# Performance work log

Measured on AMD Instinct MI355X. Metric: run time of the kernel, lower is better.

## Reference

```python
import jax, jax.numpy as jnp
import numpy as np

N = 50000      # nodes
E = 800000     # edges (avg degree 16)
D_IN = 128
D_H = 128
D_OUT = 8


def setup_inputs() -> dict:
    key = jax.random.key(0)
    ks = jax.random.split(key, 12)
    def lin(k, fan_in, shape):
        return (jax.random.normal(k, shape, jnp.float32) / np.float32(np.sqrt(fan_in)))
    return {
        "node_features": jax.random.normal(ks[0], (N, D_IN), jnp.float32),
        "edge_index": jax.random.randint(ks[1], (2, E), 0, N, jnp.int32),
        # 3 GCNConv layers: weight [in, out] + bias [out]
        "W0": lin(ks[2], D_IN, (D_IN, D_H)), "b0": jnp.zeros((D_H,), jnp.float32),
        "W1": lin(ks[3], D_H, (D_H, D_H)),  "b1": jnp.zeros((D_H,), jnp.float32),
        "W2": lin(ks[4], D_H, (D_H, D_H)),  "b2": jnp.zeros((D_H,), jnp.float32),
        # classifier MLP: hidden -> hidden//2 -> output
        "cW1": lin(ks[5], D_H, (D_H, D_H // 2)), "cb1": jnp.zeros((D_H // 2,), jnp.float32),
        "cW2": lin(ks[6], D_H // 2, (D_H // 2, D_OUT)), "cb2": jnp.zeros((D_OUT,), jnp.float32),
    }


def _gcn_norm(edge_index, n):
    # PyG GCNConv default: add self-loops, symmetric D^-1/2 (A+I) D^-1/2 normalization
    loops = jnp.arange(n, dtype=edge_index.dtype)
    src = jnp.concatenate([edge_index[0], loops])   # message sources j
    dst = jnp.concatenate([edge_index[1], loops])   # aggregation targets i
    deg = jax.ops.segment_sum(jnp.ones_like(src, dtype=jnp.float32), dst, num_segments=n)
    dinv = jax.lax.rsqrt(jnp.maximum(deg, 1.0))     # deg >= 1 due to self-loops
    norm = dinv[src] * dinv[dst]                    # [E+N]
    return src, dst, norm


def _gcn_conv(x, W, b, src, dst, norm, n):
    h = x @ W                                        # [N, out] dense transform first (PyG order)
    msg = h[src] * norm[:, None]                     # gather + scale  [E+N, out]
    out = jax.ops.segment_sum(msg, dst, num_segments=n)  # scatter-add
    return out + b


def reference(node_features, edge_index, W0, b0, W1, b1, W2, b2, cW1, cb1, cW2, cb2):
    n = node_features.shape[0]
    src, dst, norm = _gcn_norm(edge_index, n)
    x = jax.nn.relu(_gcn_conv(node_features, W0, b0, src, dst, norm, n))  # dropout is identity in eval
    x = jax.nn.relu(_gcn_conv(x, W1, b1, src, dst, norm, n))
    x = _gcn_conv(x, W2, b2, src, dst, norm, n)       # last conv: no relu/dropout
    # classifier MLP (dropout identity in eval)
    h = jax.nn.relu(x @ cW1 + cb1)
    return h @ cW2 + cb2                              # [N, D_OUT]
```

## Files before the change

### kernel.cpp

```cpp
#include <hip/hip_runtime.h>
#include <hip/hip_fp16.h>


#define CAP 48
#define FPG 256

using half8v  = __attribute__((ext_vector_type(8))) _Float16;
using float4v = __attribute__((ext_vector_type(4))) float;

__global__ __launch_bounds__(256) void fill_kernel(const int* __restrict__ src,
                                                   const int* __restrict__ dst, int e, int n,
                                                   const float* __restrict__ W0,
                                                   const float* __restrict__ W1,
                                                   const float* __restrict__ W2,
                                                   const float* __restrict__ cW1,
                                                   const float* __restrict__ cb1,
                                                   const float* __restrict__ b2,
                                                   int* __restrict__ cnt,
                                                   unsigned short* __restrict__ col,
                                                   __half* __restrict__ Wf0,
                                                   __half* __restrict__ Wf1,
                                                   __half* __restrict__ Wfc,
                                                   float* __restrict__ bc) {
    int b = blockIdx.x;
    int tid = threadIdx.x;
    const int FILLB = 8 * FPG;
    if (b < FILLB) {
        int g = b & 7;
        int cb = b >> 3;
        int npp = (n + 7) >> 3;
        int lo = g * npp;
        int hi = min(lo + npp, n);
        int step = FPG * 256;
        for (int i = cb * 256 + tid; i < e; i += step) {
            int d = dst[i];
            int s = src[i];
            if (d >= lo && d < hi) {
                int c = atomicAdd(&cnt[d], 1);
                if (c < CAP) col[d * CAP + c] = (unsigned short)s;
            }
        }
        return;
    }
    b -= FILLB;
    if (b < 16) {
        int t = b * 256 + tid;
        const float* W = (t < 2048) ? W0 : W1;
        __half* Wf = (t < 2048) ? Wf0 : Wf1;
        int u = t & 2047;
        int lane = u & 63, tile = (u >> 6) & 7, kk = u >> 9;
        int k0 = kk * 32 + (lane >> 4) * 8;
        int nn = tile * 16 + (lane & 15);
        __half tmp[8];
        #pragma unroll
        for (int j = 0; j < 8; j++) tmp[j] = __float2half(W[(k0 + j) * 128 + nn]);
        *(float4*)(Wf + (size_t)u * 8) = *(const float4*)tmp;
        return;
    }
    b -= 16;
    if (b < 4) {
        int u = b * 256 + tid;
        int lane = u & 63, tile = (u >> 6) & 3, kk = u >> 8;
        int k0 = kk * 32 + (lane >> 4) * 8;
        int nn = tile * 16 + (lane & 15);
        float a[8] = {};
        for (int m = 0; m < 128; m++) {
            float c = cW1[m * 64 + nn];
            #pragma unroll
            for (int j = 0; j < 8; j++) a[j] = fmaf(W2[(k0 + j) * 128 + m], c, a[j]);
        }
        __half tmp[8];
        #pragma unroll
        for (int j = 0; j < 8; j++) tmp[j] = __float2half(a[j]);
        *(float4*)(Wfc + (size_t)u * 8) = *(const float4*)tmp;
        return;
    }
    if (tid < 64) {
        float a = cb1[tid];
        for (int k = 0; k < 128; k++) a = fmaf(b2[k], cW1[k * 64 + tid], a);
        bc[tid] = a;
    }
}

__global__ __launch_bounds__(256) void gemm0_mfma(const float* __restrict__ x,
                                                  const __half* __restrict__ Wf,
                                                  const int* __restrict__ cnt,
                                                  __half* __restrict__ out, int n) {
    int tid = threadIdx.x;
    int wv = tid >> 6, lane = tid & 63;
    int row0 = blockIdx.x * 64 + wv * 16;
    int m = lane & 15, q = lane >> 4;
    int ra = min(row0 + m, n - 1);
    const float* xrow = x + (size_t)ra * 128 + q * 8;
    const _Float16* wf = (const _Float16*)Wf + (size_t)lane * 8;
    float4v acc[8] = {};
    #pragma unroll
    for (int kk = 0; kk < 4; kk++) {
        float4 xa = *(const float4*)(xrow + kk * 32);
        float4 xb = *(const float4*)(xrow + kk * 32 + 4);
        half8v a;
        a[0] = (_Float16)xa.x; a[1] = (_Float16)xa.y;
        a[2] = (_Float16)xa.z; a[3] = (_Float16)xa.w;
        a[4] = (_Float16)xb.x; a[5] = (_Float16)xb.y;
        a[6] = (_Float16)xb.z; a[7] = (_Float16)xb.w;
        #pragma unroll
        for (int t8 = 0; t8 < 8; t8++) {
            half8v bfr = *(const half8v*)(wf + (size_t)(kk * 8 + t8) * 512);
            acc[t8] = __builtin_amdgcn_mfma_f32_16x16x32_f16(a, bfr, acc[t8], 0, 0, 0);
        }
    }
    int rowv[4];
    float dr[4];
    #pragma unroll
    for (int r = 0; r < 4; r++) {
        rowv[r] = row0 + q * 4 + r;
        dr[r] = (rowv[r] < n) ? rsqrtf((float)(cnt[rowv[r]] + 1)) : 0.f;
    }
    #pragma unroll
    for (int t8 = 0; t8 < 8; t8++) {
        #pragma unroll
        for (int r = 0; r < 4; r++) {
            if (rowv[r] < n)
                out[(size_t)t8 * n * 16 + (size_t)rowv[r] * 16 + m] =
                    __float2half(acc[t8][r] * dr[r]);
        }
    }
}

__global__ __launch_bounds__(256) void gemm_mfma(const __half* __restrict__ x,
                                                 const __half* __restrict__ Wf,
                                                 const int* __restrict__ cnt,
                                                 __half* __restrict__ out, int n) {
    int tid = threadIdx.x;
    int wv = tid >> 6, lane = tid & 63;
    int row0 = blockIdx.x * 64 + wv * 16;
    int m = lane & 15, q = lane >> 4;
    int ra = min(row0 + m, n - 1);
    const _Float16* xb = (const _Float16*)x;
    const _Float16* wf = (const _Float16*)Wf + (size_t)lane * 8;
    float4v acc[8] = {};
    #pragma unroll
    for (int kk = 0; kk < 4; kk++) {
        int tki = kk * 2 + (q >> 1);
        half8v a = *(const half8v*)(xb + (size_t)tki * n * 16 + (size_t)ra * 16 + (q & 1) * 8);
        #pragma unroll
        for (int t8 = 0; t8 < 8; t8++) {
            half8v bfr = *(const half8v*)(wf + (size_t)(kk * 8 + t8) * 512);
            acc[t8] = __builtin_amdgcn_mfma_f32_16x16x32_f16(a, bfr, acc[t8], 0, 0, 0);
        }
    }
    int rowv[4];
    float dr[4];
    #pragma unroll
    for (int r = 0; r < 4; r++) {
        rowv[r] = row0 + q * 4 + r;
        dr[r] = (rowv[r] < n) ? rsqrtf((float)(cnt[rowv[r]] + 1)) : 0.f;
    }
    #pragma unroll
    for (int t8 = 0; t8 < 8; t8++) {
        #pragma unroll
        for (int r = 0; r < 4; r++) {
            if (rowv[r] < n)
                out[(size_t)t8 * n * 16 + (size_t)rowv[r] * 16 + m] =
                    __float2half(acc[t8][r] * dr[r]);
        }
    }
}

__global__ __launch_bounds__(256) void agg_tiled(const __half* __restrict__ hin,
                                                 const int* __restrict__ cnt,
                                                 const unsigned short* __restrict__ col,
                                                 const float* __restrict__ bias,
                                                 __half* __restrict__ hout,
                                                 int n, int relu, int scale_out) {
    int ft = blockIdx.x & 7;
    int nb = blockIdx.x >> 3;
    int tid = threadIdx.x;
    int node = nb * 128 + (tid >> 1);
    int hf = tid & 1;
    int ic = min(node, n - 1);
    const _Float16* hsl = (const _Float16*)hin + (size_t)ft * n * 16 + hf * 8;
    int ci = cnt[ic];
    int len = min(ci, CAP);
    float di = rsqrtf((float)(ci + 1));
    half8v s = *(const half8v*)(hsl + (size_t)ic * 16);
    float acc[8];
    #pragma unroll
    for (int t = 0; t < 8; t++) acc[t] = (float)s[t];
    const unsigned short* crow = col + ic * CAP;
    for (int k0 = 0; k0 < len; k0 += 4) {
        uint2 c8 = *(const uint2*)(crow + k0);
        int j[4];
        j[0] = c8.x & 0xffff; j[1] = c8.x >> 16;
        j[2] = c8.y & 0xffff; j[3] = c8.y >> 16;
        float w[4];
        half8v v[4];
        #pragma unroll
        for (int u = 0; u < 4; u++) {
            bool val = (k0 + u) < len;
            w[u] = val ? 1.f : 0.f;
            int jj = val ? j[u] : ic;
            v[u] = *(const half8v*)(hsl + (size_t)jj * 16);
        }
        #pragma unroll
        for (int u = 0; u < 4; u++) {
            #pragma unroll
            for (int t = 0; t < 8; t++) acc[t] = fmaf(w[u], (float)v[u][t], acc[t]);
        }
    }
    if (node < n) {
        float post = scale_out ? di : 1.f;
        half8v o;
        #pragma unroll
        for (int t = 0; t < 8; t++) {
            float bv = bias ? bias[ft * 16 + hf * 8 + t] : 0.f;
            float a = fmaf(acc[t], di, bv);
            if (relu) a = fmaxf(a, 0.f);
            o[t] = (_Float16)(a * post);
        }
        *(half8v*)((_Float16*)hout + (size_t)ft * n * 16 + (size_t)node * 16 + hf * 8) = o;
    }
}

__global__ __launch_bounds__(256) void gemmc_cls(const __half* __restrict__ g,
                                                 const __half* __restrict__ Wfc,
                                                 const float* __restrict__ bc,
                                                 const float* __restrict__ cW2,
                                                 const float* __restrict__ cb2,
                                                 float* __restrict__ out, int n) {
    __shared__ float hs[64 * 65];
    int tid = threadIdx.x;
    int wv = tid >> 6, lane = tid & 63;
    int row0 = blockIdx.x * 64 + wv * 16;
    int m = lane & 15, q = lane >> 4;
    int ra = min(row0 + m, n - 1);
    const _Float16* xb = (const _Float16*)g;
    const _Float16* wf = (const _Float16*)Wfc + (size_t)lane * 8;
    float4v acc[4] = {};
    #pragma unroll
    for (int kk = 0; kk < 4; kk++) {
        int tki = kk * 2 + (q >> 1);
        half8v a = *(const half8v*)(xb + (size_t)tki * n * 16 + (size_t)ra * 16 + (q & 1) * 8);
        #pragma unroll
        for (int t8 = 0; t8 < 4; t8++) {
            half8v bfr = *(const half8v*)(wf + (size_t)(kk * 4 + t8) * 512);
            acc[t8] = __builtin_amdgcn_mfma_f32_16x16x32_f16(a, bfr, acc[t8], 0, 0, 0);
        }
    }
    #pragma unroll
    for (int t8 = 0; t8 < 4; t8++) {
        float bb = bc[t8 * 16 + m];
        #pragma unroll
        for (int r = 0; r < 4; r++) {
            int rl = wv * 16 + q * 4 + r;
            hs[rl * 65 + t8 * 16 + m] = fmaxf(acc[t8][r] + bb, 0.f);
        }
    }
    __syncthreads();
    #pragma unroll
    for (int p = 0; p < 2; p++) {
        int idx = p * 256 + tid;
        int rl = idx >> 3, c2 = idx & 7;
        int row = blockIdx.x * 64 + rl;
        if (row < n) {
            float a = cb2[c2];
            const float* hr = &hs[rl * 65];
            #pragma unroll 8
            for (int k = 0; k < 64; k++) a = fmaf(hr[k], cW2[k * 8 + c2], a);
            out[row * 8 + c2] = a;
        }
    }
}

extern "C" void kernel_launch(void* const* d_in, const int* in_sizes, int n_in,
                              void* d_out, int out_size, void* d_ws, size_t ws_size,
                              hipStream_t stream) {
    const float* x   = (const float*)d_in[0];
    const int*   ei  = (const int*)d_in[1];
    const float* W0  = (const float*)d_in[2];
    const float* b0  = (const float*)d_in[3];
    const float* W1  = (const float*)d_in[4];
    const float* b1  = (const float*)d_in[5];
    const float* W2  = (const float*)d_in[6];
    const float* b2  = (const float*)d_in[7];
    const float* cW1 = (const float*)d_in[8];
    const float* cb1 = (const float*)d_in[9];
    const float* cW2 = (const float*)d_in[10];
    const float* cb2 = (const float*)d_in[11];
    float* out = (float*)d_out;

    int N = in_sizes[0] / 128;
    int E = in_sizes[1] / 2;
    const int* src = ei;
    const int* dst = ei + E;

    char* ws = (char*)d_ws;
    size_t off = 0;
    auto alloc = [&](size_t bytes) {
        void* p = ws + off;
        off = (off + bytes + 255) & ~(size_t)255;
        return p;
    };
    int* cnt              = (int*)alloc((size_t)N * 4);
    unsigned short* col   = (unsigned short*)alloc((size_t)N * CAP * 2);
    __half* Wf0           = (__half*)alloc((size_t)128 * 128 * 2);
    __half* Wf1           = (__half*)alloc((size_t)128 * 128 * 2);
    __half* Wfc           = (__half*)alloc((size_t)128 * 64 * 2);
    float* bc             = (float*)alloc(64 * 4);
    __half* hA            = (__half*)alloc((size_t)N * 128 * 2);
    __half* hB            = (__half*)alloc((size_t)N * 128 * 2);

    hipMemsetAsync(cnt, 0, (size_t)N * 4, stream);

    fill_kernel<<<8 * FPG + 21, 256, 0, stream>>>(src, dst, E, N, W0, W1, W2,
                                                  cW1, cb1, b2,
                                                  cnt, col, Wf0, Wf1, Wfc, bc);

    int NBLK = (N + 63) / 64;
    int ABLK = ((N + 127) / 128) * 8;
    gemm0_mfma<<<NBLK, 256, 0, stream>>>(x, Wf0, cnt, hA, N);
    agg_tiled<<<ABLK, 256, 0, stream>>>(hA, cnt, col, b0, hB, N, 1, 0);
    gemm_mfma<<<NBLK, 256, 0, stream>>>(hB, Wf1, cnt, hA, N);
    agg_tiled<<<ABLK, 256, 0, stream>>>(hA, cnt, col, b1, hB, N, 1, 1);
    agg_tiled<<<ABLK, 256, 0, stream>>>(hB, cnt, col, (const float*)0, hA, N, 0, 0);
    gemmc_cls<<<NBLK, 256, 0, stream>>>(hA, Wfc, bc, cW2, cb2, out, N);
}
```

Baseline: 288.5 us.

## Widen feature tiles to 32 halves and unroll neighbor gather by eight

The intermediate feature layout changes from 8 tiles of 16 halves to 4 tiles of 32 halves per node. Each neighbor gather now reads a contiguous 64-byte segment shared by four threads instead of 32 bytes shared by two. The GEMM store and load indexing and the aggregation grid are updated to match. The aggregation loop is unrolled to 8 neighbors per iteration with a single 16-byte column-index load, and the edge reads in the fill pass become nontemporal loads. The wider tiles mean fewer feature passes over the column list and better use of memory transactions, at the cost of more registers and more padding waste for low-degree nodes.

```diff
diff --git a/kernel.cpp b/kernel.cpp
--- a/kernel.cpp
+++ b/kernel.cpp
@@ -33,8 +33,8 @@
         int hi = min(lo + npp, n);
         int step = FPG * 256;
         for (int i = cb * 256 + tid; i < e; i += step) {
-            int d = dst[i];
-            int s = src[i];
+            int d = __builtin_nontemporal_load(dst + i);
+            int s = __builtin_nontemporal_load(src + i);
             if (d >= lo && d < hi) {
                 int c = atomicAdd(&cnt[d], 1);
                 if (c < CAP) col[d * CAP + c] = (unsigned short)s;
@@ -121,7 +121,7 @@
         #pragma unroll
         for (int r = 0; r < 4; r++) {
             if (rowv[r] < n)
-                out[(size_t)t8 * n * 16 + (size_t)rowv[r] * 16 + m] =
+                out[(size_t)(t8 >> 1) * n * 32 + (size_t)rowv[r] * 32 + (t8 & 1) * 16 + m] =
                     __float2half(acc[t8][r] * dr[r]);
         }
     }
@@ -142,7 +142,8 @@
     #pragma unroll
     for (int kk = 0; kk < 4; kk++) {
         int tki = kk * 2 + (q >> 1);
-        half8v a = *(const half8v*)(xb + (size_t)tki * n * 16 + (size_t)ra * 16 + (q & 1) * 8);
+        half8v a = *(const half8v*)(xb + (size_t)(tki >> 1) * n * 32 + (size_t)ra * 32 +
+                                    (tki & 1) * 16 + (q & 1) * 8);
         #pragma unroll
         for (int t8 = 0; t8 < 8; t8++) {
             half8v bfr = *(const half8v*)(wf + (size_t)(kk * 8 + t8) * 512);
@@ -161,7 +162,7 @@
         #pragma unroll
         for (int r = 0; r < 4; r++) {
             if (rowv[r] < n)
-                out[(size_t)t8 * n * 16 + (size_t)rowv[r] * 16 + m] =
+                out[(size_t)(t8 >> 1) * n * 32 + (size_t)rowv[r] * 32 + (t8 & 1) * 16 + m] =
                     __float2half(acc[t8][r] * dr[r]);
         }
     }
@@ -173,37 +174,39 @@
                                                  const float* __restrict__ bias,
                                                  __half* __restrict__ hout,
                                                  int n, int relu, int scale_out) {
-    int ft = blockIdx.x & 7;
-    int nb = blockIdx.x >> 3;
-    int tid = threadIdx.x;
-    int node = nb * 128 + (tid >> 1);
-    int hf = tid & 1;
+    int ft = blockIdx.x & 3;
+    int nb = blockIdx.x >> 2;
+    int tid = threadIdx.x;
+    int node = nb * 64 + (tid >> 2);
+    int q = tid & 3;
     int ic = min(node, n - 1);
-    const _Float16* hsl = (const _Float16*)hin + (size_t)ft * n * 16 + hf * 8;
+    const _Float16* hsl = (const _Float16*)hin + (size_t)ft * n * 32 + q * 8;
     int ci = cnt[ic];
     int len = min(ci, CAP);
     float di = rsqrtf((float)(ci + 1));
-    half8v s = *(const half8v*)(hsl + (size_t)ic * 16);
+    half8v s = *(const half8v*)(hsl + (size_t)ic * 32);
     float acc[8];
     #pragma unroll
     for (int t = 0; t < 8; t++) acc[t] = (float)s[t];
     const unsigned short* crow = col + ic * CAP;
-    for (int k0 = 0; k0 < len; k0 += 4) {
-        uint2 c8 = *(const uint2*)(crow + k0);
-        int j[4];
-        j[0] = c8.x & 0xffff; j[1] = c8.x >> 16;
-        j[2] = c8.y & 0xffff; j[3] = c8.y >> 16;
-        float w[4];
-        half8v v[4];
-        #pragma unroll
-        for (int u = 0; u < 4; u++) {
+    for (int k0 = 0; k0 < len; k0 += 8) {
+        uint4 c16 = *(const uint4*)(crow + k0);
+        int j[8];
+        j[0] = c16.x & 0xffff; j[1] = c16.x >> 16;
+        j[2] = c16.y & 0xffff; j[3] = c16.y >> 16;
+        j[4] = c16.z & 0xffff; j[5] = c16.z >> 16;
+        j[6] = c16.w & 0xffff; j[7] = c16.w >> 16;
+        float w[8];
+        half8v v[8];
+        #pragma unroll
+        for (int u = 0; u < 8; u++) {
             bool val = (k0 + u) < len;
             w[u] = val ? 1.f : 0.f;
             int jj = val ? j[u] : ic;
-            v[u] = *(const half8v*)(hsl + (size_t)jj * 16);
-        }
-        #pragma unroll
-        for (int u = 0; u < 4; u++) {
+            v[u] = *(const half8v*)(hsl + (size_t)jj * 32);
+        }
+        #pragma unroll
+        for (int u = 0; u < 8; u++) {
             #pragma unroll
             for (int t = 0; t < 8; t++) acc[t] = fmaf(w[u], (float)v[u][t], acc[t]);
         }
@@ -213,12 +216,12 @@
         half8v o;
         #pragma unroll
         for (int t = 0; t < 8; t++) {
-            float bv = bias ? bias[ft * 16 + hf * 8 + t] : 0.f;
+            float bv = bias ? bias[ft * 32 + q * 8 + t] : 0.f;
             float a = fmaf(acc[t], di, bv);
             if (relu) a = fmaxf(a, 0.f);
             o[t] = (_Float16)(a * post);
         }
-        *(half8v*)((_Float16*)hout + (size_t)ft * n * 16 + (size_t)node * 16 + hf * 8) = o;
+        *(half8v*)((_Float16*)hout + (size_t)ft * n * 32 + (size_t)node * 32 + q * 8) = o;
     }
 }
 
@@ -240,7 +243,8 @@
     #pragma unroll
     for (int kk = 0; kk < 4; kk++) {
         int tki = kk * 2 + (q >> 1);
-        half8v a = *(const half8v*)(xb + (size_t)tki * n * 16 + (size_t)ra * 16 + (q & 1) * 8);
+        half8v a = *(const half8v*)(xb + (size_t)(tki >> 1) * n * 32 + (size_t)ra * 32 +
+                                    (tki & 1) * 16 + (q & 1) * 8);
         #pragma unroll
         for (int t8 = 0; t8 < 4; t8++) {
             half8v bfr = *(const half8v*)(wf + (size_t)(kk * 4 + t8) * 512);
@@ -317,7 +321,7 @@
                                                   cnt, col, Wf0, Wf1, Wfc, bc);
 
     int NBLK = (N + 63) / 64;
-    int ABLK = ((N + 127) / 128) * 8;
+    int ABLK = ((N + 63) / 64) * 4;
     gemm0_mfma<<<NBLK, 256, 0, stream>>>(x, Wf0, cnt, hA, N);
     agg_tiled<<<ABLK, 256, 0, stream>>>(hA, cnt, col, b0, hB, N, 1, 0);
     gemm_mfma<<<NBLK, 256, 0, stream>>>(hB, Wf1, cnt, hA, N);
```

Result: faster. 258.2 us (-10.5%).
